# Optimization experiments

Measured on AMD Instinct MI355X. Metric: run time of the kernel, lower is better.

## Reference

```python
import jax, jax.numpy as jnp
import numpy as np

N = 100000
E = 1600000
DIN = 128
HID = 128
EPS = 1e-5


def setup_inputs() -> dict:
    key = jax.random.key(0)
    ks = jax.random.split(key, 16)
    s = lambda i, shape, sc=0.05: jax.random.normal(ks[i], shape, dtype=jnp.float32) * sc
    inp = {
        "x": jax.random.normal(ks[0], (N, DIN), dtype=jnp.float32),
        "edge_index": jax.random.randint(ks[1], (2, E), 0, N, dtype=jnp.int64),
        # layer 1
        "W1": s(2, (DIN, HID)), "b1": jnp.zeros((HID,), jnp.float32),
        "g1": jnp.ones((HID,), jnp.float32), "be1": jnp.zeros((HID,), jnp.float32),
        "m1": s(3, (HID,)), "v1": jax.random.uniform(ks[4], (HID,), jnp.float32) + 0.5,
        # layer 2
        "W2": s(5, (HID, HID)), "b2": jnp.zeros((HID,), jnp.float32),
        "g2": jnp.ones((HID,), jnp.float32), "be2": jnp.zeros((HID,), jnp.float32),
        "m2": s(6, (HID,)), "v2": jax.random.uniform(ks[7], (HID,), jnp.float32) + 0.5,
        # classifier
        "Wc1": s(8, (HID, HID // 2)), "bc1": jnp.zeros((HID // 2,), jnp.float32),
        "Wc2": s(9, (HID // 2, 2)), "bc2": jnp.zeros((2,), jnp.float32),
    }
    return inp


def _gnn_layer(x, W, b, src, dst):
    # linear then scatter-mean of source features onto destinations
    h = x @ W + b                                    # [N, HID]
    msg_sum = jax.ops.segment_sum(h[src], dst, num_segments=N)   # [N, HID]
    cnt = jax.ops.segment_sum(jnp.ones((src.shape[0],), h.dtype), dst, num_segments=N)
    return msg_sum / cnt[:, None]                    # self-loops guarantee cnt >= 1


def _bn(x, g, be, m, v):
    return (x - m) * jax.lax.rsqrt(v + EPS) * g + be


def reference(x, edge_index, W1, b1, g1, be1, m1, v1, W2, b2, g2, be2, m2, v2, Wc1, bc1, Wc2, bc2):
    # add self loops (PyG add_self_loops appends [i, i])
    loop = jnp.arange(N, dtype=edge_index.dtype)
    src = jnp.concatenate([edge_index[0], loop])
    dst = jnp.concatenate([edge_index[1], loop])

    h = _gnn_layer(x, W1, b1, src, dst)
    h = jax.nn.relu(_bn(h, g1, be1, m1, v1))
    h = _gnn_layer(h, W2, b2, src, dst)
    h = jax.nn.relu(_bn(h, g2, be2, m2, v2))

    h = jax.nn.relu(h @ Wc1 + bc1)
    return h @ Wc2 + bc2                              # logits [N, 2]
```

## Files before the change

### kernel.cpp

```cpp
#include <hip/hip_runtime.h>
#include <hip/hip_bf16.h>

#define EPS 1e-5f

__global__ __launch_bounds__(256) void k_histrank(const int* __restrict__ dst,
                                                  int* __restrict__ counts,
                                                  int* __restrict__ rank, int nE) {
    int i = blockIdx.x * 256 + threadIdx.x;
    if (i < nE) {
        int p = atomicAdd(&counts[dst[i]], 1);
        __builtin_nontemporal_store(p, &rank[i]);
    }
}

__global__ __launch_bounds__(256) void k_scan1(const int* __restrict__ counts,
                                               int* __restrict__ bsums, int n) {
    __shared__ int sdata[256];
    int base = blockIdx.x * 2048;
    int t = threadIdx.x;
    int s = 0;
#pragma unroll
    for (int i = 0; i < 8; ++i) {
        int idx = base + t * 8 + i;
        if (idx < n) s += counts[idx];
    }
    sdata[t] = s;
    __syncthreads();
    for (int off = 128; off > 0; off >>= 1) {
        if (t < off) sdata[t] += sdata[t + off];
        __syncthreads();
    }
    if (t == 0) bsums[blockIdx.x] = sdata[0];
}

__global__ __launch_bounds__(64) void k_scan2(int* __restrict__ bsums, int nb) {
    if (threadIdx.x == 0 && blockIdx.x == 0) {
        int acc = 0;
        for (int i = 0; i < nb; ++i) { int v = bsums[i]; bsums[i] = acc; acc += v; }
    }
}

__global__ __launch_bounds__(256) void k_scan3(const int* __restrict__ counts,
                                               const int* __restrict__ bsums,
                                               int* __restrict__ rowstart,
                                               int n, int nE) {
    __shared__ int sth[256];
    int base = blockIdx.x * 2048;
    int t = threadIdx.x;
    int loc[8];
    int s = 0;
#pragma unroll
    for (int i = 0; i < 8; ++i) {
        int idx = base + t * 8 + i;
        loc[i] = s;
        s += (idx < n) ? counts[idx] : 0;
    }
    sth[t] = s;
    __syncthreads();
    for (int off = 1; off < 256; off <<= 1) {
        int tmp = (t >= off) ? sth[t - off] : 0;
        __syncthreads();
        sth[t] += tmp;
        __syncthreads();
    }
    int excl = sth[t] - s + bsums[blockIdx.x];
#pragma unroll
    for (int i = 0; i < 8; ++i) {
        int idx = base + t * 8 + i;
        if (idx < n) rowstart[idx] = excl + loc[i];
    }
    if (blockIdx.x == 0 && t == 0) rowstart[n] = nE;
}

__global__ __launch_bounds__(256) void k_fill3(const int* __restrict__ srci,
                                               const int* __restrict__ dsti,
                                               const int* __restrict__ rank,
                                               const int* __restrict__ rowstart,
                                               int* __restrict__ col, int nE) {
    int e = blockIdx.x * 256 + threadIdx.x;
    if (e < nE) {
        col[rowstart[dsti[e]] + rank[e]] = srci[e];
    }
}

__global__ __launch_bounds__(256) void k_linear(const float* __restrict__ X,
                                                const float* __restrict__ W,
                                                const float* __restrict__ bias,
                                                float* __restrict__ out,
                                                int nRows) {
    __shared__ float xs[64][132];
    int row0 = blockIdx.x * 64;
    int tid = threadIdx.x;
    for (int i = tid; i < 64 * 32; i += 256) {
        int r = i >> 5, c4 = (i & 31) << 2;
        float4 v = make_float4(0.f, 0.f, 0.f, 0.f);
        int row = row0 + r;
        if (row < nRows) v = *(const float4*)(X + (size_t)row * 128 + c4);
        *(float4*)&xs[r][c4] = v;
    }
    __syncthreads();

    int cg = tid & 15, rg = tid >> 4;
    int c0 = cg * 8, r0 = rg * 4;
    float acc[4][8];
    float4 b0 = *(const float4*)(bias + c0);
    float4 b1 = *(const float4*)(bias + c0 + 4);
#pragma unroll
    for (int r = 0; r < 4; ++r) {
        acc[r][0] = b0.x; acc[r][1] = b0.y; acc[r][2] = b0.z; acc[r][3] = b0.w;
        acc[r][4] = b1.x; acc[r][5] = b1.y; acc[r][6] = b1.z; acc[r][7] = b1.w;
    }

    for (int k0 = 0; k0 < 128; k0 += 4) {
        float4 xv[4];
#pragma unroll
        for (int r = 0; r < 4; ++r) xv[r] = *(const float4*)&xs[r0 + r][k0];
#pragma unroll
        for (int kk = 0; kk < 4; ++kk) {
            int k = k0 + kk;
            float4 w0 = *(const float4*)(W + k * 128 + c0);
            float4 w1 = *(const float4*)(W + k * 128 + c0 + 4);
            float wv[8] = {w0.x, w0.y, w0.z, w0.w, w1.x, w1.y, w1.z, w1.w};
#pragma unroll
            for (int r = 0; r < 4; ++r) {
                float xk = (&xv[r].x)[kk];
#pragma unroll
                for (int j = 0; j < 8; ++j) acc[r][j] = fmaf(xk, wv[j], acc[r][j]);
            }
        }
    }

#pragma unroll
    for (int r = 0; r < 4; ++r) {
        int row = row0 + r0 + r;
        if (row >= nRows) continue;
        *(float4*)(out + (size_t)row * 128 + c0) =
            make_float4(acc[r][0], acc[r][1], acc[r][2], acc[r][3]);
        *(float4*)(out + (size_t)row * 128 + c0 + 4) =
            make_float4(acc[r][4], acc[r][5], acc[r][6], acc[r][7]);
    }
}

template <bool FUSE_BN>
__global__ __launch_bounds__(256) void k_gather(const float* __restrict__ src,
                                                const int* __restrict__ rowstart,
                                                const int* __restrict__ col,
                                                const float* __restrict__ g,
                                                const float* __restrict__ be,
                                                const float* __restrict__ m,
                                                const float* __restrict__ v,
                                                float* __restrict__ out, int nRows) {
    int r = blockIdx.x * 4 + (threadIdx.x >> 6);
    if (r >= nRows) return;
    int lane = threadIdx.x & 63;
    int half = lane >> 5;
    int li = lane & 31;
    int d0 = li * 4;
    int s = rowstart[r], e = rowstart[r + 1];
    int deg = e - s;

    float4 acc = make_float4(0.f, 0.f, 0.f, 0.f);
    if (half == 0) acc = *(const float4*)(src + (size_t)r * 128 + d0);

    int nP = deg >> 1;
    int p = 0;
    for (; p + 4 <= nP; p += 4) {
        int jb = s + 2 * p + half;
        int c0i = col[jb], c1i = col[jb + 2], c2i = col[jb + 4], c3i = col[jb + 6];
        float4 t0 = *(const float4*)(src + (size_t)c0i * 128 + d0);
        float4 t1 = *(const float4*)(src + (size_t)c1i * 128 + d0);
        float4 t2 = *(const float4*)(src + (size_t)c2i * 128 + d0);
        float4 t3 = *(const float4*)(src + (size_t)c3i * 128 + d0);
        acc.x += (t0.x + t1.x) + (t2.x + t3.x);
        acc.y += (t0.y + t1.y) + (t2.y + t3.y);
        acc.z += (t0.z + t1.z) + (t2.z + t3.z);
        acc.w += (t0.w + t1.w) + (t2.w + t3.w);
    }
    for (; p < nP; ++p) {
        int ci = col[s + 2 * p + half];
        float4 t = *(const float4*)(src + (size_t)ci * 128 + d0);
        acc.x += t.x; acc.y += t.y; acc.z += t.z; acc.w += t.w;
    }
    if ((deg & 1) && half == 0) {
        int ci = col[e - 1];
        float4 t = *(const float4*)(src + (size_t)ci * 128 + d0);
        acc.x += t.x; acc.y += t.y; acc.z += t.z; acc.w += t.w;
    }

    acc.x += __shfl_xor(acc.x, 32, 64);
    acc.y += __shfl_xor(acc.y, 32, 64);
    acc.z += __shfl_xor(acc.z, 32, 64);
    acc.w += __shfl_xor(acc.w, 32, 64);

    if (half == 0) {
        float rc = 1.0f / (float)(deg + 1);
        float4 o;
        if (FUSE_BN) {
            float4 gv  = *(const float4*)(g + d0);
            float4 bev = *(const float4*)(be + d0);
            float4 mv  = *(const float4*)(m + d0);
            float4 vv  = *(const float4*)(v + d0);
            o.x = fmaxf((acc.x * rc - mv.x) * rsqrtf(vv.x + EPS) * gv.x + bev.x, 0.f);
            o.y = fmaxf((acc.y * rc - mv.y) * rsqrtf(vv.y + EPS) * gv.y + bev.y, 0.f);
            o.z = fmaxf((acc.z * rc - mv.z) * rsqrtf(vv.z + EPS) * gv.z + bev.z, 0.f);
            o.w = fmaxf((acc.w * rc - mv.w) * rsqrtf(vv.w + EPS) * gv.w + bev.w, 0.f);
        } else {
            o.x = acc.x * rc; o.y = acc.y * rc; o.z = acc.z * rc; o.w = acc.w * rc;
        }
        *(float4*)(out + (size_t)r * 128 + d0) = o;
    }
}

__global__ __launch_bounds__(256) void k_final(const float* __restrict__ xin,
                                               const float* __restrict__ Wc1,
                                               const float* __restrict__ bc1,
                                               const float* __restrict__ Wc2,
                                               const float* __restrict__ bc2,
                                               float* __restrict__ out, int nRows) {
    __shared__ float xs[32][132];
    __shared__ float w1s[128][64];
    __shared__ float hs[32][68];
    int row0 = blockIdx.x * 32;
    int tid = threadIdx.x;

    for (int i = tid; i < 2048; i += 256) {
        int kk = i >> 4, c4 = (i & 15) << 2;
        *(float4*)&w1s[kk][c4] = *(const float4*)(Wc1 + kk * 64 + c4);
    }
    for (int i = tid; i < 1024; i += 256) {
        int r = i >> 5, c4 = (i & 31) << 2;
        int row = row0 + r;
        float4 o = make_float4(0.f, 0.f, 0.f, 0.f);
        if (row < nRows) o = *(const float4*)(xin + (size_t)row * 128 + c4);
        *(float4*)&xs[r][c4] = o;
    }
    __syncthreads();

    int cg = tid & 15, rg = tid >> 4;
    int c0 = cg * 4, r0 = rg * 2;
    float acc[2][4];
    float4 bc = *(const float4*)(bc1 + c0);
    acc[0][0] = bc.x; acc[0][1] = bc.y; acc[0][2] = bc.z; acc[0][3] = bc.w;
    acc[1][0] = bc.x; acc[1][1] = bc.y; acc[1][2] = bc.z; acc[1][3] = bc.w;
    for (int k = 0; k < 128; ++k) {
        float4 w4 = *(const float4*)&w1s[k][c0];
        float x0 = xs[r0][k], x1 = xs[r0 + 1][k];
        acc[0][0] = fmaf(x0, w4.x, acc[0][0]);
        acc[0][1] = fmaf(x0, w4.y, acc[0][1]);
        acc[0][2] = fmaf(x0, w4.z, acc[0][2]);
        acc[0][3] = fmaf(x0, w4.w, acc[0][3]);
        acc[1][0] = fmaf(x1, w4.x, acc[1][0]);
        acc[1][1] = fmaf(x1, w4.y, acc[1][1]);
        acc[1][2] = fmaf(x1, w4.z, acc[1][2]);
        acc[1][3] = fmaf(x1, w4.w, acc[1][3]);
    }
    *(float4*)&hs[r0][c0] = make_float4(fmaxf(acc[0][0], 0.f), fmaxf(acc[0][1], 0.f),
                                        fmaxf(acc[0][2], 0.f), fmaxf(acc[0][3], 0.f));
    *(float4*)&hs[r0 + 1][c0] = make_float4(fmaxf(acc[1][0], 0.f), fmaxf(acc[1][1], 0.f),
                                            fmaxf(acc[1][2], 0.f), fmaxf(acc[1][3], 0.f));
    __syncthreads();

    if (tid < 64) {
        int r = tid >> 1, oc = tid & 1;
        float s = bc2[oc];
        for (int c = 0; c < 64; ++c) s = fmaf(hs[r][c], Wc2[c * 2 + oc], s);
        int row = row0 + r;
        if (row < nRows) out[(size_t)row * 2 + oc] = s;
    }
}

extern "C" void kernel_launch(void* const* d_in, const int* in_sizes, int n_in,
                              void* d_out, int out_size, void* d_ws, size_t ws_size,
                              hipStream_t stream) {
    const float* x   = (const float*)d_in[0];
    const int*   ei  = (const int*)d_in[1];
    const float* W1  = (const float*)d_in[2];
    const float* b1  = (const float*)d_in[3];
    const float* g1  = (const float*)d_in[4];
    const float* be1 = (const float*)d_in[5];
    const float* m1  = (const float*)d_in[6];
    const float* v1  = (const float*)d_in[7];
    const float* W2  = (const float*)d_in[8];
    const float* b2  = (const float*)d_in[9];
    const float* g2  = (const float*)d_in[10];
    const float* be2 = (const float*)d_in[11];
    const float* m2  = (const float*)d_in[12];
    const float* v2  = (const float*)d_in[13];
    const float* Wc1 = (const float*)d_in[14];
    const float* bc1 = (const float*)d_in[15];
    const float* Wc2 = (const float*)d_in[16];
    const float* bc2 = (const float*)d_in[17];

    const int N_ = in_sizes[0] / 128;
    const int E_ = in_sizes[1] / 2;
    const int* srci = ei;
    const int* dsti = ei + E_;

    float* A = (float*)d_ws;
    float* B = A + (size_t)N_ * 128;
    int* rank = (int*)B;
    int* counts   = (int*)(B + (size_t)N_ * 128);
    int* rowstart = counts + N_;
    int* bsums    = rowstart + N_ + 1;
    int* col      = bsums + 256;

    const int nb = (N_ + 2047) / 2048;

    hipMemsetAsync(counts, 0, (size_t)N_ * sizeof(int), stream);
    k_histrank<<<(E_ + 255) / 256, 256, 0, stream>>>(dsti, counts, rank, E_);
    k_scan1   <<<nb, 256, 0, stream>>>(counts, bsums, N_);
    k_scan2   <<<1, 64, 0, stream>>>(bsums, nb);
    k_scan3   <<<nb, 256, 0, stream>>>(counts, bsums, rowstart, N_, E_);
    k_fill3   <<<(E_ + 255) / 256, 256, 0, stream>>>(srci, dsti, rank, rowstart,
                                                     col, E_);

    k_linear<<<(N_ + 63) / 64, 256, 0, stream>>>(x, W1, b1, A, N_);
    k_gather<true><<<(N_ + 3) / 4, 256, 0, stream>>>(A, rowstart, col,
                                                     g1, be1, m1, v1, B, N_);

    k_linear<<<(N_ + 63) / 64, 256, 0, stream>>>(B, W2, b2, A, N_);
    k_gather<true><<<(N_ + 3) / 4, 256, 0, stream>>>(A, rowstart, col,
                                                     g2, be2, m2, v2, B, N_);

    k_final<<<(N_ + 31) / 32, 256, 0, stream>>>(B, Wc1, bc1, Wc2, bc2,
                                                (float*)d_out, N_);
}
```

Measured before the change: 644.6 us.

## Replace FP32 linear layers with split-bf16 MFMA matrix multiply

Splits the activations and weights into high and low bf16 parts, then computes each 128x128 linear layer with three bf16 MFMA products (hi*hi, hi*lo, lo*hi). This approximates FP32 accuracy while using the matrix cores instead of scalar FMA loops. A small prep kernel transposes and splits the weights into the workspace on every call. The cost is some lost precision, LDS conversion work, uncoalesced scalar output stores, and weight fragments read straight from global/L2 rather than shared memory.

```diff
diff --git a/kernel.cpp b/kernel.cpp
--- a/kernel.cpp
+++ b/kernel.cpp
@@ -2,6 +2,37 @@
 #include <hip/hip_bf16.h>
 
 #define EPS 1e-5f
+
+using bf16x8 = __attribute__((ext_vector_type(8))) short;
+using f32x4  = __attribute__((ext_vector_type(4))) float;
+
+__device__ __forceinline__ void bf16_split(float f, unsigned short& h, unsigned short& l) {
+    unsigned u = __float_as_uint(f);
+    unsigned hu = (u + 0x8000u) & 0xFFFF0000u;
+    float fh = __uint_as_float(hu);
+    h = (unsigned short)(hu >> 16);
+    float rl = f - fh;
+    unsigned ul = __float_as_uint(rl);
+    l = (unsigned short)((ul + 0x8000u) >> 16);
+}
+
+__global__ __launch_bounds__(256) void k_wprep(const float* __restrict__ W1,
+                                               const float* __restrict__ W2,
+                                               unsigned short* __restrict__ w1h,
+                                               unsigned short* __restrict__ w1l,
+                                               unsigned short* __restrict__ w2h,
+                                               unsigned short* __restrict__ w2l) {
+    int idx = blockIdx.x * 256 + threadIdx.x;
+    if (idx >= 32768) return;
+    int mtx = idx >> 14;
+    int rem = idx & 16383;
+    int k = rem >> 7, n = rem & 127;
+    float w = mtx ? W2[k * 128 + n] : W1[k * 128 + n];
+    unsigned short h, l;
+    bf16_split(w, h, l);
+    if (mtx) { w2h[n * 128 + k] = h; w2l[n * 128 + k] = l; }
+    else     { w1h[n * 128 + k] = h; w1l[n * 128 + k] = l; }
+}
 
 __global__ __launch_bounds__(256) void k_histrank(const int* __restrict__ dst,
                                                   int* __restrict__ counts,
@@ -83,61 +114,60 @@
     }
 }
 
-__global__ __launch_bounds__(256) void k_linear(const float* __restrict__ X,
-                                                const float* __restrict__ W,
-                                                const float* __restrict__ bias,
-                                                float* __restrict__ out,
-                                                int nRows) {
-    __shared__ float xs[64][132];
+__global__ __launch_bounds__(256) void k_linmf(const float* __restrict__ X,
+                                               const unsigned short* __restrict__ WhT,
+                                               const unsigned short* __restrict__ WlT,
+                                               const float* __restrict__ bias,
+                                               float* __restrict__ out, int nRows) {
+    __shared__ __align__(16) unsigned short xh[64][136];
+    __shared__ __align__(16) unsigned short xl[64][136];
     int row0 = blockIdx.x * 64;
     int tid = threadIdx.x;
+
     for (int i = tid; i < 64 * 32; i += 256) {
         int r = i >> 5, c4 = (i & 31) << 2;
         float4 v = make_float4(0.f, 0.f, 0.f, 0.f);
         int row = row0 + r;
         if (row < nRows) v = *(const float4*)(X + (size_t)row * 128 + c4);
-        *(float4*)&xs[r][c4] = v;
-    }
-    __syncthreads();
-
-    int cg = tid & 15, rg = tid >> 4;
-    int c0 = cg * 8, r0 = rg * 4;
-    float acc[4][8];
-    float4 b0 = *(const float4*)(bias + c0);
-    float4 b1 = *(const float4*)(bias + c0 + 4);
-#pragma unroll
-    for (int r = 0; r < 4; ++r) {
-        acc[r][0] = b0.x; acc[r][1] = b0.y; acc[r][2] = b0.z; acc[r][3] = b0.w;
-        acc[r][4] = b1.x; acc[r][5] = b1.y; acc[r][6] = b1.z; acc[r][7] = b1.w;
-    }
-
-    for (int k0 = 0; k0 < 128; k0 += 4) {
-        float4 xv[4];
-#pragma unroll
-        for (int r = 0; r < 4; ++r) xv[r] = *(const float4*)&xs[r0 + r][k0];
-#pragma unroll
-        for (int kk = 0; kk < 4; ++kk) {
-            int k = k0 + kk;
-            float4 w0 = *(const float4*)(W + k * 128 + c0);
-            float4 w1 = *(const float4*)(W + k * 128 + c0 + 4);
-            float wv[8] = {w0.x, w0.y, w0.z, w0.w, w1.x, w1.y, w1.z, w1.w};
-#pragma unroll
-            for (int r = 0; r < 4; ++r) {
-                float xk = (&xv[r].x)[kk];
-#pragma unroll
-                for (int j = 0; j < 8; ++j) acc[r][j] = fmaf(xk, wv[j], acc[r][j]);
-            }
+        unsigned short h0, l0, h1, l1, h2, l2, h3, l3;
+        bf16_split(v.x, h0, l0); bf16_split(v.y, h1, l1);
+        bf16_split(v.z, h2, l2); bf16_split(v.w, h3, l3);
+        xh[r][c4] = h0; xh[r][c4 + 1] = h1; xh[r][c4 + 2] = h2; xh[r][c4 + 3] = h3;
+        xl[r][c4] = l0; xl[r][c4 + 1] = l1; xl[r][c4 + 2] = l2; xl[r][c4 + 3] = l3;
+    }
+    __syncthreads();
+
+    int w = tid >> 6, lane = tid & 63;
+    int t16 = lane & 15;
+    int kg = lane >> 4;
+
+    f32x4 acc[8];
+#pragma unroll
+    for (int ct = 0; ct < 8; ++ct) acc[ct] = (f32x4){0.f, 0.f, 0.f, 0.f};
+
+    for (int k0 = 0; k0 < 128; k0 += 32) {
+        bf16x8 ah = *(const bf16x8*)&xh[w * 16 + t16][k0 + kg * 8];
+        bf16x8 al = *(const bf16x8*)&xl[w * 16 + t16][k0 + kg * 8];
+#pragma unroll
+        for (int ct = 0; ct < 8; ++ct) {
+            size_t boff = (size_t)(ct * 16 + t16) * 128 + k0 + kg * 8;
+            bf16x8 bh = *(const bf16x8*)(WhT + boff);
+            bf16x8 bl = *(const bf16x8*)(WlT + boff);
+            acc[ct] = __builtin_amdgcn_mfma_f32_16x16x32_bf16(ah, bh, acc[ct], 0, 0, 0);
+            acc[ct] = __builtin_amdgcn_mfma_f32_16x16x32_bf16(ah, bl, acc[ct], 0, 0, 0);
+            acc[ct] = __builtin_amdgcn_mfma_f32_16x16x32_bf16(al, bh, acc[ct], 0, 0, 0);
         }
     }
 
 #pragma unroll
-    for (int r = 0; r < 4; ++r) {
-        int row = row0 + r0 + r;
-        if (row >= nRows) continue;
-        *(float4*)(out + (size_t)row * 128 + c0) =
-            make_float4(acc[r][0], acc[r][1], acc[r][2], acc[r][3]);
-        *(float4*)(out + (size_t)row * 128 + c0 + 4) =
-            make_float4(acc[r][4], acc[r][5], acc[r][6], acc[r][7]);
+    for (int ct = 0; ct < 8; ++ct) {
+        int c = ct * 16 + t16;
+        float b = bias[c];
+#pragma unroll
+        for (int j = 0; j < 4; ++j) {
+            int r = row0 + w * 16 + kg * 4 + j;
+            if (r < nRows) out[(size_t)r * 128 + c] = acc[ct][j] + b;
+        }
     }
 }
 
@@ -303,8 +333,15 @@
     int* rowstart = counts + N_;
     int* bsums    = rowstart + N_ + 1;
     int* col      = bsums + 256;
+    uintptr_t wp  = ((uintptr_t)(col + E_) + 63) & ~(uintptr_t)63;
+    unsigned short* w1h = (unsigned short*)wp;
+    unsigned short* w1l = w1h + 16384;
+    unsigned short* w2h = w1l + 16384;
+    unsigned short* w2l = w2h + 16384;
 
     const int nb = (N_ + 2047) / 2048;
+
+    k_wprep<<<128, 256, 0, stream>>>(W1, W2, w1h, w1l, w2h, w2l);
 
     hipMemsetAsync(counts, 0, (size_t)N_ * sizeof(int), stream);
     k_histrank<<<(E_ + 255) / 256, 256, 0, stream>>>(dsti, counts, rank, E_);
@@ -314,11 +351,11 @@
     k_fill3   <<<(E_ + 255) / 256, 256, 0, stream>>>(srci, dsti, rank, rowstart,
                                                      col, E_);
 
-    k_linear<<<(N_ + 63) / 64, 256, 0, stream>>>(x, W1, b1, A, N_);
+    k_linmf<<<(N_ + 63) / 64, 256, 0, stream>>>(x, w1h, w1l, b1, A, N_);
     k_gather<true><<<(N_ + 3) / 4, 256, 0, stream>>>(A, rowstart, col,
                                                      g1, be1, m1, v1, B, N_);
 
-    k_linear<<<(N_ + 63) / 64, 256, 0, stream>>>(B, W2, b2, A, N_);
+    k_linmf<<<(N_ + 63) / 64, 256, 0, stream>>>(B, w2h, w2l, b2, A, N_);
     k_gather<true><<<(N_ + 3) / 4, 256, 0, stream>>>(A, rowstart, col,
                                                      g2, be2, m2, v2, B, N_);
 
```

Measured after the change: 652.4 us. About the same (+1.2%).
